# Kernel optimization log

Hardware: AMD Instinct MI355X
Metric: run time of the kernel (lower is better)

Reference implementation:

```python
import jax, jax.numpy as jnp
from jax import lax
import numpy as np

B, H, W = 2048, 28, 28
LATENT_EACH = 64
LATENT = 2 * LATENT_EACH  # 128
MEM_SIZE = 8192
TOPK = 10
EPS = 1e-12


def _conv(x, w, b):
    # x: NCHW, w: OIHW, 3x3 conv, padding=1 (SAME)
    y = lax.conv_general_dilated(x, w, (1, 1), 'SAME',
                                 dimension_numbers=('NCHW', 'OIHW', 'NCHW'))
    return y + b[None, :, None, None]


def _deconv(x, w, b):
    # ConvTranspose2d(k=4, stride=2, padding=1) -> out = 2*in (SAME transpose)
    # w: HWIO = (4,4,in,out)
    y = lax.conv_transpose(x, w, (2, 2), 'SAME',
                           dimension_numbers=('NCHW', 'HWIO', 'NCHW'))
    return y + b[None, :, None, None]


def _encoder(x, w1, b1, w2, b2, fcw, fcb):
    h = jax.nn.relu(_conv(x, w1, b1))
    h = jax.nn.relu(_conv(h, w2, b2))
    feat = h.mean(axis=(2, 3))  # AdaptiveAvgPool2d((1,1)) + flatten -> [B,64]
    return feat @ fcw.T + fcb


def _memory_match(z, mem):
    mn = mem / jnp.maximum(jnp.linalg.norm(mem, axis=1, keepdims=True), EPS)
    zn = z / jnp.maximum(jnp.linalg.norm(z, axis=1, keepdims=True), EPS)
    sim = zn @ mn.T                      # [B, MEM_SIZE]
    topv, topi = lax.top_k(sim, TOPK)    # [B, K]
    wts = jax.nn.softmax(topv, axis=1)   # [B, K]
    sel = mem[topi]                      # gather: [B, K, LATENT]
    return jnp.einsum('bk,bkd->bd', wts, sel)


def setup_inputs() -> dict:
    key = jax.random.key(0)
    ks = jax.random.split(key, 24)
    g = lambda k, s, scale=0.05: jax.random.normal(k, s, jnp.float32) * scale
    inp = {
        'x': jax.random.normal(ks[0], (B, 1, H, W), jnp.float32),
        # center encoder
        'ce_w1': g(ks[1], (32, 1, 3, 3)), 'ce_b1': jnp.zeros((32,), jnp.float32),
        'ce_w2': g(ks[2], (64, 32, 3, 3)), 'ce_b2': jnp.zeros((64,), jnp.float32),
        'ce_fcw': g(ks[3], (LATENT_EACH, 64)), 'ce_fcb': jnp.zeros((LATENT_EACH,), jnp.float32),
        # global encoder
        'ge_w1': g(ks[4], (32, 1, 3, 3)), 'ge_b1': jnp.zeros((32,), jnp.float32),
        'ge_w2': g(ks[5], (64, 32, 3, 3)), 'ge_b2': jnp.zeros((64,), jnp.float32),
        'ge_fcw': g(ks[6], (LATENT_EACH, 64)), 'ge_fcb': jnp.zeros((LATENT_EACH,), jnp.float32),
        # memory bank (Parameter ~ randn)
        'mem': jax.random.normal(ks[7], (MEM_SIZE, LATENT), jnp.float32),
        # decoder
        'dec_fcw': g(ks[8], (64 * 7 * 7, LATENT)), 'dec_fcb': jnp.zeros((64 * 7 * 7,), jnp.float32),
        'd_w1': g(ks[9], (4, 4, 64, 32)), 'd_b1': jnp.zeros((32,), jnp.float32),   # deconv 64->32
        'd_w2': g(ks[10], (16, 32, 3, 3)), 'd_b2': jnp.zeros((16,), jnp.float32),  # conv 32->16
        'd_w3': g(ks[11], (4, 4, 16, 8)), 'd_b3': jnp.zeros((8,), jnp.float32),    # deconv 16->8
        'd_w4': g(ks[12], (1, 8, 3, 3)), 'd_b4': jnp.zeros((1,), jnp.float32),     # conv 8->1
    }
    return inp


def reference(x, ce_w1, ce_b1, ce_w2, ce_b2, ce_fcw, ce_fcb,
              ge_w1, ge_b1, ge_w2, ge_b2, ge_fcw, ge_fcb,
              mem, dec_fcw, dec_fcb,
              d_w1, d_b1, d_w2, d_b2, d_w3, d_b3, d_w4, d_b4):
    # crop_center(x, 14): start = (28-14)//2 = 7
    x_center = x[:, :, 7:21, 7:21]
    z_center = _encoder(x_center, ce_w1, ce_b1, ce_w2, ce_b2, ce_fcw, ce_fcb)
    z_global = _encoder(x, ge_w1, ge_b1, ge_w2, ge_b2, ge_fcw, ge_fcb)
    z = jnp.concatenate([z_center, z_global], axis=1)  # [B, 128]
    z_match = _memory_match(z, mem)                    # [B, 128]
    d = (z_match @ dec_fcw.T + dec_fcb).reshape(B, 64, 7, 7)
    d = jax.nn.relu(_deconv(d, d_w1, d_b1))   # [B,32,14,14]
    d = jax.nn.relu(_conv(d, d_w2, d_b2))     # [B,16,14,14]
    d = jax.nn.relu(_deconv(d, d_w3, d_b3))   # [B,8,28,28]
    x_hat = _conv(d, d_w4, d_b4)              # [B,1,28,28]
    return x_hat
```

## Files before the change

### kernel.cpp

```cpp
#include <hip/hip_runtime.h>
#include <cfloat>
#include <cmath>

#define TPB 256

typedef _Float16 half8 __attribute__((ext_vector_type(8)));
typedef float floatx16 __attribute__((ext_vector_type(16)));
typedef float floatx4 __attribute__((ext_vector_type(4)));
typedef float floatx2 __attribute__((ext_vector_type(2)));

__device__ __forceinline__ float wave_reduce_sum(float v) {
#pragma unroll
  for (int off = 32; off > 0; off >>= 1) v += __shfl_xor(v, off, 64);
  return v;
}

__global__ __launch_bounds__(64) void prep_bfrags(
    const float* __restrict__ ce_w2, const float* __restrict__ ge_w2,
    float* __restrict__ frags) {
  const int blk = blockIdx.x;
  const int enc = blk / 72;
  const int frag = blk % 72;
  const int ks = frag >> 2, part = (frag >> 1) & 1, nt = frag & 1;
  const int tap = ks >> 1, half = ks & 1;
  const int lane = threadIdx.x;
  const float* w2 = enc ? ge_w2 : ce_w2;
  const int n = nt * 32 + (lane & 31);
  const int cb = half * 16 + (lane >> 5) * 8;
  half8 out;
#pragma unroll
  for (int j = 0; j < 8; ++j) {
    float v = w2[(n * 32 + cb + j) * 9 + tap];
    _Float16 h = (_Float16)v;
    out[j] = (part == 0) ? h : (_Float16)((v - (float)h) * 4096.f);
  }
  *(half8*)((char*)frags + ((size_t)blk * 64 + lane) * 16) = out;
}

__global__ __launch_bounds__(64) void prep_dec1(
    const float* __restrict__ w1, float* __restrict__ frags) {
  const int blk = blockIdx.x;
  const int phase = blk >> 4, ks = blk & 15;
  const int pa = phase >> 1, pb = phase & 1;
  const int st = ks >> 2, kk = ks & 3;
  const int s = st >> 1, tt = st & 1;
  const int lane = threadIdx.x;
  const int kg = lane >> 5, n = lane & 31;
  const int tap = (pa + 2 * s) * 4 + (pb + 2 * tt);
  half8 o;
#pragma unroll
  for (int j = 0; j < 8; ++j) {
    int c = kk * 16 + kg * 8 + j;
    o[j] = (_Float16)w1[tap * 2048 + c * 32 + n];
  }
  *(half8*)((char*)frags + ((size_t)blk * 64 + lane) * 16) = o;
}

__global__ __launch_bounds__(64) void prep_dfc(
    const float* __restrict__ dfcw, float* __restrict__ frags) {
  const int blk = blockIdx.x;
  const int nt = blk >> 3, ks = blk & 7;
  const int lane = threadIdx.x;
  const int n = lane & 31, kg = lane >> 5;
  const int j = nt * 32 + n;
  const int px = j >> 6, c = j & 63;
  half8 o;
#pragma unroll
  for (int u = 0; u < 8; ++u)
    o[u] = (_Float16)dfcw[(size_t)(c * 49 + px) * 128 + ks * 16 + kg * 8 + u];
  *(half8*)((char*)frags + ((size_t)blk * 64 + lane) * 16) = o;
}

__global__ __launch_bounds__(64) void prep_mem(
    const float* __restrict__ memg, float* __restrict__ frags) {
  const int blk = blockIdx.x;
  const int slot = blk & 15;
  const int p = slot >> 3, ks = slot & 7;
  const int T = blk >> 4;
  const int lane = threadIdx.x;
  const int n = lane & 31, kg = lane >> 5;
  const float* src = memg + (size_t)(T * 32 + n) * 128 + ks * 16 + kg * 8;
  half8 o;
#pragma unroll
  for (int j = 0; j < 8; ++j) {
    float v = src[j];
    _Float16 h = (_Float16)v;
    o[j] = p ? (_Float16)((v - (float)h) * 4096.f) : h;
  }
  *(half8*)((char*)frags + ((size_t)blk * 64 + lane) * 16) = o;
}

__global__ __launch_bounds__(256) void norm_kernel(
    const float* __restrict__ memg, float* __restrict__ invn) {
  const int wv = threadIdx.x >> 6, lane = threadIdx.x & 63;
  const int row = blockIdx.x * 4 + wv;
  const float* r = memg + (size_t)row * 128;
  float a = r[lane], b = r[lane + 64];
  float s = wave_reduce_sum(a * a + b * b);
  if (lane == 0) invn[row] = 1.f / fmaxf(sqrtf(s), 1e-12f);
}

template <int S, bool CENTER>
__device__ __forceinline__ void encoder_body(
    char* smem, const float* __restrict__ x, const float* __restrict__ w1,
    const float* __restrict__ b1, const float* __restrict__ b2,
    const float* __restrict__ fcw, const float* __restrict__ fcb,
    const float* __restrict__ bfrag, float* __restrict__ zout, int zoff,
    int b) {
  constexpr int SP = S + 2;
  constexpr int NBANDS = (S == 28) ? 3 : 2;
  constexpr int RMAX = 12;
  constexpr int NPIX = RMAX * SP;
  constexpr int GSTB = NPIX * 16;
  constexpr int PSTB = 4 * GSTB;

  char* h1s = smem;
  float* xs = (float*)(smem + 2 * PSTB);
  float* featp = xs + SP * SP;

  const int t = threadIdx.x;
  const int lane = t & 63;
  const int wv = t >> 6;
  const int ntW = wv & 1;

  const int gbase = __builtin_amdgcn_readfirstlane(wv * 8);
  floatx2 w1p[4][9];
  floatx2 b1p[4];
#pragma unroll
  for (int up = 0; up < 4; ++up) {
    b1p[up][0] = b1[gbase + 2 * up];
    b1p[up][1] = b1[gbase + 2 * up + 1];
#pragma unroll
    for (int v = 0; v < 9; ++v) {
      w1p[up][v][0] = w1[(gbase + 2 * up) * 9 + v];
      w1p[up][v][1] = w1[(gbase + 2 * up + 1) * 9 + v];
    }
  }

  for (int e = t; e < SP * SP; e += TPB) xs[e] = 0.f;
  __syncthreads();
  const float* xb = x + (size_t)b * 784 + (CENTER ? (7 * 28 + 7) : 0);
  for (int e = t; e < S * S; e += TPB) {
    int i = e / S, j = e - i * S;
    xs[(i + 1) * SP + (j + 1)] = xb[i * 28 + j];
  }

  float sp = 0.f;
  const float biasW = b2[ntW * 32 + (lane & 31)];
  const int gOff = (lane >> 5) * GSTB;
  const char* bgbase = (const char*)bfrag + lane * 16;

#pragma unroll
  for (int band = 0; band < NBANDS; ++band) {
    const int BH_ = (S == 28) ? ((band < 2) ? 10 : 8) : ((band == 0) ? 10 : 4);
    const int b0 = band * 10;
    const int LIMIT = BH_ * S;
    const int MTB = (LIMIT + 31) / 32;

    __syncthreads();
    for (int pix = lane; pix < NPIX; pix += 64) {
      int lr = pix / SP, cw = pix - lr * SP;
      int gr = b0 - 1 + lr;
      half8 hi8 = {}, lo8 = {};
      if (gr >= 0 && gr < S && cw >= 1 && cw <= S) {
        float xv[9];
#pragma unroll
        for (int di = 0; di < 3; ++di)
#pragma unroll
          for (int dj = 0; dj < 3; ++dj)
            xv[di * 3 + dj] = xs[(gr + di) * SP + (cw - 1 + dj)];
#pragma unroll
        for (int up = 0; up < 4; ++up) {
          floatx2 a2 = b1p[up];
#pragma unroll
          for (int v = 0; v < 9; ++v) a2 += xv[v] * w1p[up][v];
#pragma unroll
          for (int q = 0; q < 2; ++q) {
            float a = fmaxf(a2[q], 0.f);
            _Float16 h = (_Float16)a;
            hi8[2 * up + q] = h;
            lo8[2 * up + q] = (_Float16)((a - (float)h) * 4096.f);
          }
        }
      }
      const int ebase = wv * GSTB + pix * 16;
      *(half8*)(h1s + ebase) = hi8;
      *(half8*)(h1s + PSTB + ebase) = lo8;
    }
    __syncthreads();
#pragma unroll 1
    for (int u = wv; u < 2 * MTB; u += 4) {
      const int mt = u >> 1;
      floatx16 accH = {}, accL = {};
      int px = mt * 32 + (lane & 31);
      px = px < LIMIT ? px : LIMIT - 1;
      const int r = px / S, cc = px - r * S;
      const int pixB = (r * SP + cc) * 16;
#pragma unroll
      for (int tap = 0; tap < 9; ++tap) {
        const int di = tap / 3, dj = tap - di * 3;
        const int offT = (di * SP + dj) * 16;
#pragma unroll
        for (int half = 0; half < 2; ++half) {
          const int ks = tap * 2 + half;
          const char* bp = bgbase + ks * 4096 + ntW * 1024;
          const int offA = pixB + offT + gOff + half * (2 * GSTB);
          half8 ah = *(const half8*)(h1s + offA);
          half8 al = *(const half8*)(h1s + PSTB + offA);
          half8 bh = *(const half8*)(bp);
          half8 bl = *(const half8*)(bp + 2048);
          accH = __builtin_amdgcn_mfma_f32_32x32x16_f16(ah, bh, accH, 0, 0, 0);
          accL = __builtin_amdgcn_mfma_f32_32x32x16_f16(ah, bl, accL, 0, 0, 0);
          accL = __builtin_amdgcn_mfma_f32_32x32x16_f16(al, bh, accL, 0, 0, 0);
        }
      }
#pragma unroll
      for (int reg = 0; reg < 16; ++reg) {
        int row = (reg & 3) + 8 * (reg >> 2) + 4 * (lane >> 5);
        int p = mt * 32 + row;
        if (p < LIMIT)
          sp += fmaxf(accH[reg] + accL[reg] * (1.f / 4096.f) + biasW, 0.f);
      }
    }
  }
  sp += __shfl_xor(sp, 32);
  if (lane < 32) featp[wv * 32 + lane] = sp;
  __syncthreads();
  if (t < 64) featp[t] = (featp[t] + featp[64 + t]) * (1.f / (S * S));
  __syncthreads();
  if (t < 64) {
    float s = 0.f;
#pragma unroll
    for (int i = 0; i < 64; ++i) s += featp[i] * fcw[t * 64 + i];
    zout[(size_t)b * 128 + zoff + t] = s + fcb[t];
  }
}

__global__ __launch_bounds__(256, 3) void encoders_fused(
    const float* __restrict__ x, const float* __restrict__ ce_w1,
    const float* __restrict__ ce_b1, const float* __restrict__ ce_b2,
    const float* __restrict__ ce_fcw, const float* __restrict__ ce_fcb,
    const float* __restrict__ ge_w1, const float* __restrict__ ge_b1,
    const float* __restrict__ ge_b2, const float* __restrict__ ge_fcw,
    const float* __restrict__ ge_fcb, const float* __restrict__ frags,
    float* __restrict__ z) {
  __shared__ __align__(16) char smem[50192];
  if (blockIdx.x < 2048)
    encoder_body<28, false>(smem, x, ge_w1, ge_b1, ge_b2, ge_fcw, ge_fcb,
                            frags + 18432, z, 64, blockIdx.x);
  else
    encoder_body<14, true>(smem, x, ce_w1, ce_b1, ce_b2, ce_fcw, ce_fcb, frags,
                           z, 0, blockIdx.x - 2048);
}

__global__ __launch_bounds__(256) void match_mfma(
    const float* __restrict__ z, const float* __restrict__ memfrags,
    const float* __restrict__ invn, float* __restrict__ topvw,
    int* __restrict__ topiw) {
  __shared__ __align__(16) char smem[49408];
  float* zs = (float*)smem;
  float* qv = (float*)smem;
  int* qi = (int*)(smem + 16384);
  char* zfrag = smem + 32768;
  float* rowmin = (float*)(smem + 49152);
  int* qn = (int*)(smem + 49152 + 128);

  const int t = threadIdx.x;
  const int lane = t & 63;
  const int wv = t >> 6;
  const int rowbase = blockIdx.x * 32;
  const int Tbase = blockIdx.y * 16;

  for (int e = t; e < 4096; e += TPB) zs[e] = z[(size_t)rowbase * 128 + e];
  if (t < 32) { rowmin[t] = -FLT_MAX; qn[t] = 0; }
  __syncthreads();
#pragma unroll
  for (int h = 0; h < 8; ++h) {
    int r = wv * 8 + h;
    float a = zs[r * 128 + lane], b = zs[r * 128 + 64 + lane];
    float s = wave_reduce_sum(a * a + b * b);
    float inv = 1.f / fmaxf(sqrtf(s), 1e-12f);
    zs[r * 128 + lane] = a * inv;
    zs[r * 128 + 64 + lane] = b * inv;
  }
  __syncthreads();
  for (int e = t; e < 4096; e += TPB) {
    int m = e >> 7, c = e & 127;
    float v = zs[m * 128 + c];
    _Float16 h = (_Float16)v;
    _Float16 l = (_Float16)((v - (float)h) * 4096.f);
    int ks = c >> 4, kg = (c >> 3) & 1, j = c & 7;
    int off = (ks * 64 + kg * 32 + m) * 16 + j * 2;
    *(_Float16*)(zfrag + off) = h;
    *(_Float16*)(zfrag + 8192 + off) = l;
  }
  __syncthreads();

  half8 ah[8], al[8];
  {
    const char* zf = zfrag + ((lane >> 5) * 32 + (lane & 31)) * 16;
#pragma unroll
    for (int ks = 0; ks < 8; ++ks) {
      ah[ks] = *(const half8*)(zf + ks * 1024);
      al[ks] = *(const half8*)(zf + 8192 + ks * 1024);
    }
  }

  float av[10];
  int ai[10];
#pragma unroll
  for (int i = 0; i < 10; ++i) { av[i] = -FLT_MAX; ai[i] = 0; }

#pragma unroll 1
  for (int round = 0; round < 4; ++round) {
    const int T = Tbase + round * 4 + wv;
    const char* bf = (const char*)memfrags + (size_t)T * 16384 + lane * 16;
    floatx16 acc0 = {}, acc1 = {};
#pragma unroll
    for (int ks = 0; ks < 8; ++ks) {
      half8 bh = *(const half8*)(bf + ks * 1024);
      half8 bl = *(const half8*)(bf + 8192 + ks * 1024);
      acc0 = __builtin_amdgcn_mfma_f32_32x32x16_f16(ah[ks], bh, acc0, 0, 0, 0);
      acc1 = __builtin_amdgcn_mfma_f32_32x32x16_f16(ah[ks], bl, acc1, 0, 0, 0);
      acc1 = __builtin_amdgcn_mfma_f32_32x32x16_f16(al[ks], bh, acc1, 0, 0, 0);
    }
    const int gn = T * 32 + (lane & 31);
    const float iv = invn[gn];
#pragma unroll
    for (int reg = 0; reg < 16; ++reg) {
      int m = (reg & 3) + 8 * (reg >> 2) + 4 * (lane >> 5);
      float v = (acc0[reg] + acc1[reg] * (1.f / 4096.f)) * iv;
      if (v > rowmin[m]) {
        int k = atomicAdd(&qn[m], 1);
        qv[m * 128 + k] = v;
        qi[m * 128 + k] = gn;
      }
    }
    __syncthreads();
    if (t < 32) {
      int n = qn[t];
      for (int k = 0; k < n; ++k) {
        float v = qv[t * 128 + k];
        int mm = qi[t * 128 + k];
        if (v > av[9]) {
#pragma unroll
          for (int i = 0; i < 10; ++i) {
            if (v > av[i]) {
              float tv = av[i]; av[i] = v; v = tv;
              int ti = ai[i]; ai[i] = mm; mm = ti;
            }
          }
        }
      }
      qn[t] = 0;
      rowmin[t] = av[9];
    }
    __syncthreads();
  }

  if (t < 32) {
    const size_t base = (size_t)(rowbase + t) * 160 + blockIdx.y * 10;
#pragma unroll
    for (int k = 0; k < 10; ++k) {
      topvw[base + k] = av[k];
      topiw[base + k] = ai[k];
    }
  }
}

__global__ __launch_bounds__(256) void match_merge(
    const float* __restrict__ topvw, const int* __restrict__ topiw,
    const float* __restrict__ memg, _Float16* __restrict__ zmf16) {
  __shared__ float topw[8][10];
  __shared__ int topidx[8][10];
  const int t = threadIdx.x;
  const int rowbase = blockIdx.x * 8;

  if (t < 8) {
    float av[10];
    int ai[10];
#pragma unroll
    for (int i = 0; i < 10; ++i) { av[i] = -FLT_MAX; ai[i] = 0; }
    const size_t base = (size_t)(rowbase + t) * 160;
    for (int c = 0; c < 160; ++c) {
      float v = topvw[base + c];
      int m = topiw[base + c];
      if (v > av[9]) {
#pragma unroll
        for (int i = 0; i < 10; ++i) {
          if (v > av[i]) {
            float tv = av[i]; av[i] = v; v = tv;
            int ti = ai[i]; ai[i] = m; m = ti;
          }
        }
      }
    }
    float e_[10], s = 0.f;
#pragma unroll
    for (int k = 0; k < 10; ++k) { e_[k] = expf(av[k]); s += e_[k]; }
    float inv = 1.f / s;
#pragma unroll
    for (int k = 0; k < 10; ++k) { topw[t][k] = e_[k] * inv; topidx[t][k] = ai[k]; }
  }
  __syncthreads();
  for (int e = t; e < 8 * 128; e += TPB) {
    int r = e >> 7, d = e & 127;
    float o = 0.f;
#pragma unroll
    for (int k = 0; k < 10; ++k)
      o += topw[r][k] * memg[(size_t)topidx[r][k] * 128 + d];
    zmf16[(size_t)(rowbase + r) * 128 + d] = (_Float16)o;
  }
}

__global__ __launch_bounds__(256) void decfc_kernel(
    const _Float16* __restrict__ zmf16, const float* __restrict__ fcb,
    const float* __restrict__ dfcfrags, _Float16* __restrict__ d0f16) {
  const int t = threadIdx.x;
  const int lane = t & 63;
  const int wv = t >> 6;
  const int r0 = blockIdx.x * 32;
  const int ntbase = blockIdx.y * 49;

  half8 a[8];
  {
    const _Float16* ap =
        zmf16 + (size_t)(r0 + (lane & 31)) * 128 + (lane >> 5) * 8;
#pragma unroll
    for (int ks = 0; ks < 8; ++ks) a[ks] = *(const half8*)(ap + ks * 16);
  }
  const char* fb = (const char*)dfcfrags + lane * 16;

  for (int nt = ntbase + wv; nt < ntbase + 49; nt += 4) {
    half8 bfr[8];
    const char* p = fb + (size_t)nt * 8192;
#pragma unroll
    for (int ks = 0; ks < 8; ++ks) bfr[ks] = *(const half8*)(p + ks * 1024);
    floatx16 acc = {};
#pragma unroll
    for (int ks = 0; ks < 8; ++ks)
      acc = __builtin_amdgcn_mfma_f32_32x32x16_f16(a[ks], bfr[ks], acc, 0, 0, 0);
    const int col = nt * 32 + (lane & 31);
    const int px = col >> 6, c = col & 63;
    const float bias = fcb[c * 49 + px];
#pragma unroll
    for (int reg = 0; reg < 16; ++reg) {
      int row = (reg & 3) + 8 * (reg >> 2) + 4 * (lane >> 5);
      d0f16[((size_t)(r0 + row) * 49 + px) * 64 + c] = (_Float16)(acc[reg] + bias);
    }
  }
}

__global__ __launch_bounds__(256) void decoder_kernel(
    const _Float16* __restrict__ d0f16, const float* __restrict__ b1,
    const float* __restrict__ w2, const float* __restrict__ b2,
    const float* __restrict__ w3, const float* __restrict__ b3,
    const float* __restrict__ w4, const float* __restrict__ b4,
    const float* __restrict__ dec1frags, float* __restrict__ out) {
  __shared__ __align__(16) char dsm[41408];
  char* d0f = dsm;
  float* d2 = (float*)dsm;
  char* d1f = dsm + 12608;
  char* w2s = dsm + 28992;
  float* d3 = (float*)(dsm + 12608);

  const int b = blockIdx.x;
  const int t = threadIdx.x;
  const int lane = t & 63;
  const int wv = t >> 6;

  for (int e = t; e < 648; e += TPB) {
    int g = e / 81, pix = e - g * 81;
    int ih = pix / 9 - 1, iw = pix % 9 - 1;
    half8 hv = {};
    if (ih >= 0 && ih < 7 && iw >= 0 && iw < 7)
      hv = *(const half8*)(d0f16 + ((size_t)b * 49 + ih * 7 + iw) * 64 + g * 8);
    *(half8*)(d0f + e * 16) = hv;
  }
  for (int e = t; e < 576; e += TPB) {
    int tau = e / 64, l = e - tau * 64;
    int n = l & 15, kq = l >> 4;
    half8 v;
#pragma unroll
    for (int u = 0; u < 8; ++u)
      v[u] = (_Float16)w2[(n * 32 + kq * 8 + u) * 9 + tau];
    *(half8*)(w2s + e * 16) = v;
  }
  for (int e = t; e < 1024; e += TPB)
    *(float4*)(d1f + e * 16) = make_float4(0.f, 0.f, 0.f, 0.f);
  __syncthreads();

  {
    const int pa = wv >> 1, pb = wv & 1;
    const int kg = lane >> 5, o = lane & 31;
    const char* bg = (const char*)dec1frags + wv * 16384 + lane * 16;
    int pxa[2][4];
#pragma unroll
    for (int im = 0; im < 2; ++im) {
      int px = im * 32 + o;
      px = px < 49 ? px : 48;
      int i = px / 7, j2 = px - i * 7;
#pragma unroll
      for (int st = 0; st < 4; ++st) {
        int s = st >> 1, tt = st & 1;
        pxa[im][st] = ((i + pa + s) * 9 + (j2 + pb + tt)) * 16;
      }
    }
    floatx16 acc0 = {}, acc1 = {};
    half8 nb = *(const half8*)(bg);
#pragma unroll
    for (int ks = 0; ks < 16; ++ks) {
      half8 bf = nb;
      if (ks < 15) nb = *(const half8*)(bg + (ks + 1) * 1024);
      const int gbase = (((ks & 3) * 2 + kg) * 81) * 16;
      half8 a0 = *(const half8*)(d0f + gbase + pxa[0][ks >> 2]);
      half8 a1 = *(const half8*)(d0f + gbase + pxa[1][ks >> 2]);
      acc0 = __builtin_amdgcn_mfma_f32_32x32x16_f16(a0, bf, acc0, 0, 0, 0);
      acc1 = __builtin_amdgcn_mfma_f32_32x32x16_f16(a1, bf, acc1, 0, 0, 0);
    }
    const float bias = b1[o];
    char* dst = d1f + (o >> 3) * 4096 + (o & 7) * 2;
#pragma unroll
    for (int im = 0; im < 2; ++im) {
      const floatx16& ac = im ? acc1 : acc0;
#pragma unroll
      for (int reg = 0; reg < 16; ++reg) {
        int row = (reg & 3) + 8 * (reg >> 2) + 4 * kg;
        int px = im * 32 + row;
        if (px < 49) {
          int i = px / 7, j2 = px - i * 7;
          int p = 2 * i + pa, q = 2 * j2 + pb;
          *(_Float16*)(dst + ((p + 1) * 16 + (q + 1)) * 16) =
              (_Float16)fmaxf(ac[reg] + bias, 0.f);
        }
      }
    }
  }
  __syncthreads();

  {
    const int m = lane & 15, kq = lane >> 4;
    half8 bq[9];
#pragma unroll
    for (int tau = 0; tau < 9; ++tau)
      bq[tau] = *(const half8*)(w2s + (tau * 64 + lane) * 16);
    for (int mt = wv; mt < 13; mt += 4) {
      int px = mt * 16 + m;
      px = px < 196 ? px : 195;
      const int p = px / 14, q = px - (px / 14) * 14;
      floatx4 acc = {};
#pragma unroll
      for (int tau = 0; tau < 9; ++tau) {
        const int dp = tau / 3, dq = tau - dp * 3;
        half8 av =
            *(const half8*)(d1f + (kq * 256 + (p + dp) * 16 + (q + dq)) * 16);
        acc = __builtin_amdgcn_mfma_f32_16x16x32_f16(av, bq[tau], acc, 0, 0, 0);
      }
      const int o = lane & 15;
      const float bias = b2[o];
#pragma unroll
      for (int reg = 0; reg < 4; ++reg) {
        int row = (lane >> 4) * 4 + reg;
        int opx = mt * 16 + row;
        if (opx < 196) d2[o * 197 + opx] = fmaxf(acc[reg] + bias, 0.f);
      }
    }
  }
  __syncthreads();
  for (int e = t; e < 7200; e += TPB) d3[e] = 0.f;
  __syncthreads();

  {
    const int ph = __builtin_amdgcn_readfirstlane(t >> 6);
    const int pa = ph >> 1, pb = ph & 1;
    const int tb = pa * 4 + pb;
    const float* wA = w3 + (size_t)tb * 128;
    const float* wB = w3 + (size_t)(tb + 2) * 128;
    const float* wC = w3 + (size_t)(tb + 8) * 128;
    const float* wD = w3 + (size_t)(tb + 10) * 128;
#pragma unroll 1
    for (int k = 0; k < 4; ++k) {
      const int px = lane + 64 * k;
      const int cpx = px < 196 ? px : 195;
      const int i = cpx / 14, j = cpx % 14;
      int ih[2], iw[2];
      float mh[2], mw[2];
#pragma unroll
      for (int s = 0; s < 2; ++s) {
        int v = i + pa + s - 1;
        mh[s] = (v >= 0 && v <= 13) ? 1.f : 0.f;
        ih[s] = v < 0 ? 0 : (v > 13 ? 13 : v);
        int u = j + pb + s - 1;
        mw[s] = (u >= 0 && u <= 13) ? 1.f : 0.f;
        iw[s] = u < 0 ? 0 : (u > 13 ? 13 : u);
      }
      const float m00 = mh[0] * mw[0], m01 = mh[0] * mw[1];
      const float m10 = mh[1] * mw[0], m11 = mh[1] * mw[1];
      float acc[8];
#pragma unroll
      for (int oo = 0; oo < 8; ++oo) acc[oo] = b3[oo];
#pragma unroll 2
      for (int c = 0; c < 16; ++c) {
        const float a00 = d2[c * 197 + ih[0] * 14 + iw[0]] * m00;
        const float a01 = d2[c * 197 + ih[0] * 14 + iw[1]] * m01;
        const float a10 = d2[c * 197 + ih[1] * 14 + iw[0]] * m10;
        const float a11 = d2[c * 197 + ih[1] * 14 + iw[1]] * m11;
        const int wb = c * 8;
#pragma unroll
        for (int oo = 0; oo < 8; ++oo)
          acc[oo] += a00 * wA[wb + oo] + a01 * wB[wb + oo] +
                     a10 * wC[wb + oo] + a11 * wD[wb + oo];
      }
      if (px < 196) {
        const int p = 2 * i + pa, q = 2 * j + pb;
        const int widx = (p + 1) * 30 + (q + 1);
#pragma unroll
        for (int oo = 0; oo < 8; ++oo)
          d3[oo * 900 + widx] = fmaxf(acc[oo], 0.f);
      }
    }
  }
  __syncthreads();

  for (int e = t; e < 784; e += TPB) {
    int p = e / 28, q = e - p * 28;
    float a = b4[0];
#pragma unroll
    for (int c = 0; c < 8; ++c) {
      const float* bp = &d3[c * 900 + p * 30 + q];
#pragma unroll
      for (int di = 0; di < 3; ++di)
#pragma unroll
        for (int dj = 0; dj < 3; ++dj)
          a += bp[di * 30 + dj] * w4[c * 9 + di * 3 + dj];
    }
    out[(size_t)b * 784 + e] = a;
  }
}

extern "C" void kernel_launch(void* const* d_in, const int* in_sizes, int n_in,
                              void* d_out, int out_size, void* d_ws,
                              size_t ws_size, hipStream_t stream) {
  const float* x      = (const float*)d_in[0];
  const float* ce_w1  = (const float*)d_in[1];
  const float* ce_b1  = (const float*)d_in[2];
  const float* ce_w2  = (const float*)d_in[3];
  const float* ce_b2  = (const float*)d_in[4];
  const float* ce_fcw = (const float*)d_in[5];
  const float* ce_fcb = (const float*)d_in[6];
  const float* ge_w1  = (const float*)d_in[7];
  const float* ge_b1  = (const float*)d_in[8];
  const float* ge_w2  = (const float*)d_in[9];
  const float* ge_b2  = (const float*)d_in[10];
  const float* ge_fcw = (const float*)d_in[11];
  const float* ge_fcb = (const float*)d_in[12];
  const float* memg   = (const float*)d_in[13];
  const float* dfcw   = (const float*)d_in[14];
  const float* dfcb   = (const float*)d_in[15];
  const float* d_w1   = (const float*)d_in[16];
  const float* d_b1   = (const float*)d_in[17];
  const float* d_w2   = (const float*)d_in[18];
  const float* d_b2   = (const float*)d_in[19];
  const float* d_w3   = (const float*)d_in[20];
  const float* d_b3   = (const float*)d_in[21];
  const float* d_w4   = (const float*)d_in[22];
  const float* d_b4   = (const float*)d_in[23];
  float* outp = (float*)d_out;

  float*     ws        = (float*)d_ws;
  float*     z         = ws;
  _Float16*  zmf16     = (_Float16*)(ws + 262144);
  float*     invn      = ws + 262144 + 131072;
  float*     frags     = invn + 8192;
  float*     dec1frags = frags + 36864;
  float*     dfcfrags  = dec1frags + 16384;
  float*     memfrags  = dfcfrags + 200704;
  float*     tailbase  = memfrags + 1048576;
  float*     topvw     = tailbase;
  int*       topiw     = (int*)(tailbase + 327680);
  _Float16*  d0f16     = (_Float16*)tailbase;

  prep_bfrags<<<144, 64, 0, stream>>>(ce_w2, ge_w2, frags);
  prep_dec1<<<64, 64, 0, stream>>>(d_w1, dec1frags);
  prep_dfc<<<784, 64, 0, stream>>>(dfcw, dfcfrags);
  prep_mem<<<4096, 64, 0, stream>>>(memg, memfrags);
  norm_kernel<<<2048, TPB, 0, stream>>>(memg, invn);
  encoders_fused<<<4096, TPB, 0, stream>>>(x, ce_w1, ce_b1, ce_b2, ce_fcw,
                                           ce_fcb, ge_w1, ge_b1, ge_b2, ge_fcw,
                                           ge_fcb, frags, z);
  match_mfma<<<dim3(64, 16), TPB, 0, stream>>>(z, memfrags, invn, topvw, topiw);
  match_merge<<<256, TPB, 0, stream>>>(topvw, topiw, memg, zmf16);
  decfc_kernel<<<dim3(64, 2), TPB, 0, stream>>>(zmf16, dfcb, dfcfrags, d0f16);
  decoder_kernel<<<2048, TPB, 0, stream>>>(d0f16, d_b1, d_w2, d_b2, d_w3, d_b3,
                                           d_w4, d_b4, dec1frags, outp);
}
```

Baseline: 723.3 us.

## Stage conv1 weights in LDS and partially unroll the conv2 MFMA tap loop

The encoder's first-conv weights, previously held as 72 per-thread packed registers, are now copied into shared memory and read from LDS inside the pixel loop. Work is redistributed so every thread covers all four channel groups through a flat loop over 4*NPIX entries. The 9-tap MFMA loop is only partially unrolled (by 3). Together these cut register pressure so the 3-blocks-per-CU launch bound fits without spills, at the cost of extra LDS reads, scalar bias loads, and lost packed-FMA arithmetic in the conv1 stage.

```diff
diff --git a/kernel.cpp b/kernel.cpp
--- a/kernel.cpp
+++ b/kernel.cpp
@@ -7,7 +7,6 @@
 typedef _Float16 half8 __attribute__((ext_vector_type(8)));
 typedef float floatx16 __attribute__((ext_vector_type(16)));
 typedef float floatx4 __attribute__((ext_vector_type(4)));
-typedef float floatx2 __attribute__((ext_vector_type(2)));
 
 __device__ __forceinline__ float wave_reduce_sum(float v) {
 #pragma unroll
@@ -116,28 +115,16 @@
 
   char* h1s = smem;
   float* xs = (float*)(smem + 2 * PSTB);
-  float* featp = xs + SP * SP;
+  float* w1s = xs + SP * SP;
+  float* featp = w1s + 288;
 
   const int t = threadIdx.x;
   const int lane = t & 63;
   const int wv = t >> 6;
   const int ntW = wv & 1;
 
-  const int gbase = __builtin_amdgcn_readfirstlane(wv * 8);
-  floatx2 w1p[4][9];
-  floatx2 b1p[4];
-#pragma unroll
-  for (int up = 0; up < 4; ++up) {
-    b1p[up][0] = b1[gbase + 2 * up];
-    b1p[up][1] = b1[gbase + 2 * up + 1];
-#pragma unroll
-    for (int v = 0; v < 9; ++v) {
-      w1p[up][v][0] = w1[(gbase + 2 * up) * 9 + v];
-      w1p[up][v][1] = w1[(gbase + 2 * up + 1) * 9 + v];
-    }
-  }
-
   for (int e = t; e < SP * SP; e += TPB) xs[e] = 0.f;
+  for (int e = t; e < 288; e += TPB) w1s[e] = w1[e];
   __syncthreads();
   const float* xb = x + (size_t)b * 784 + (CENTER ? (7 * 28 + 7) : 0);
   for (int e = t; e < S * S; e += TPB) {
@@ -158,9 +145,13 @@
     const int MTB = (LIMIT + 31) / 32;
 
     __syncthreads();
-    for (int pix = lane; pix < NPIX; pix += 64) {
-      int lr = pix / SP, cw = pix - lr * SP;
+    for (int e = t; e < 4 * NPIX; e += TPB) {
+      int g = e / NPIX;
+      int pix = e - g * NPIX;
+      int lr = pix / SP;
+      int cw = pix - lr * SP;
       int gr = b0 - 1 + lr;
+      int ebase = g * GSTB + pix * 16;
       half8 hi8 = {}, lo8 = {};
       if (gr >= 0 && gr < S && cw >= 1 && cw <= S) {
         float xv[9];
@@ -170,20 +161,17 @@
           for (int dj = 0; dj < 3; ++dj)
             xv[di * 3 + dj] = xs[(gr + di) * SP + (cw - 1 + dj)];
 #pragma unroll
-        for (int up = 0; up < 4; ++up) {
-          floatx2 a2 = b1p[up];
-#pragma unroll
-          for (int v = 0; v < 9; ++v) a2 += xv[v] * w1p[up][v];
-#pragma unroll
-          for (int q = 0; q < 2; ++q) {
-            float a = fmaxf(a2[q], 0.f);
-            _Float16 h = (_Float16)a;
-            hi8[2 * up + q] = h;
-            lo8[2 * up + q] = (_Float16)((a - (float)h) * 4096.f);
-          }
+        for (int u = 0; u < 8; ++u) {
+          int ch = g * 8 + u;
+          float a = b1[ch];
+#pragma unroll
+          for (int v = 0; v < 9; ++v) a += xv[v] * w1s[ch * 9 + v];
+          a = fmaxf(a, 0.f);
+          _Float16 h = (_Float16)a;
+          hi8[u] = h;
+          lo8[u] = (_Float16)((a - (float)h) * 4096.f);
         }
       }
-      const int ebase = wv * GSTB + pix * 16;
       *(half8*)(h1s + ebase) = hi8;
       *(half8*)(h1s + PSTB + ebase) = lo8;
     }
@@ -196,7 +184,7 @@
       px = px < LIMIT ? px : LIMIT - 1;
       const int r = px / S, cc = px - r * S;
       const int pixB = (r * SP + cc) * 16;
-#pragma unroll
+#pragma unroll 3
       for (int tap = 0; tap < 9; ++tap) {
         const int di = tap / 3, dj = tap - di * 3;
         const int offT = (di * SP + dj) * 16;
@@ -244,7 +232,7 @@
     const float* __restrict__ ge_b2, const float* __restrict__ ge_fcw,
     const float* __restrict__ ge_fcb, const float* __restrict__ frags,
     float* __restrict__ z) {
-  __shared__ __align__(16) char smem[50192];
+  __shared__ __align__(16) char smem[51344];
   if (blockIdx.x < 2048)
     encoder_body<28, false>(smem, x, ge_w1, ge_b1, ge_b2, ge_fcw, ge_fcb,
                             frags + 18432, z, 64, blockIdx.x);
```

Result: faster. 661.3 us (-8.6%).
